# Optimization experiments

Measured on AMD Instinct MI355X. Metric: run time of the kernel, lower is better.

Reference implementation:

```python
import jax, jax.numpy as jnp
import numpy as np
from jax import lax

WINDOW_SIZE = 11
SIGMA = 1.5
CHANNELS = 3
C1 = 0.01 ** 2
C2 = 0.03 ** 2


def _create_window():
    coords = jnp.arange(WINDOW_SIZE, dtype=jnp.float32) - WINDOW_SIZE // 2
    g = jnp.exp(-coords ** 2 / (2.0 * SIGMA ** 2))
    g = g / g.sum()
    w2d = g[:, None] * g[None, :]                      # (11, 11)
    # depthwise kernel, OIHW with groups=channels -> (C, 1, k, k)
    return jnp.broadcast_to(w2d, (CHANNELS, 1, WINDOW_SIZE, WINDOW_SIZE))


def _dwconv(x, window):
    pad = WINDOW_SIZE // 2
    return lax.conv_general_dilated(
        x, window,
        window_strides=(1, 1),
        padding=[(pad, pad), (pad, pad)],
        dimension_numbers=('NCHW', 'OIHW', 'NCHW'),
        feature_group_count=CHANNELS,
    )


def setup_inputs() -> dict:
    key = jax.random.key(0)
    k1, k2 = jax.random.split(key)
    pred = jax.random.uniform(k1, (32, 3, 512, 512), dtype=jnp.float32)
    target = jax.random.uniform(k2, (32, 3, 512, 512), dtype=jnp.float32)
    return {"pred": pred, "target": target}


def reference(pred, target):
    pred = pred.astype(jnp.float32)
    target = target.astype(jnp.float32)
    window = _create_window()

    mu1 = _dwconv(pred, window)
    mu2 = _dwconv(target, window)
    mu1_sq = mu1 * mu1
    mu2_sq = mu2 * mu2
    mu1_mu2 = mu1 * mu2
    sigma1_sq = _dwconv(pred * pred, window) - mu1_sq
    sigma2_sq = _dwconv(target * target, window) - mu2_sq
    sigma12 = _dwconv(pred * target, window) - mu1_mu2

    ssim_map = ((2.0 * mu1_mu2 + C1) * (2.0 * sigma12 + C2)) / (
        (mu1_sq + mu2_sq + C1) * (sigma1_sq + sigma2_sq + C2))
    return 1.0 - ssim_map.mean()
```

## Files before the change

### kernel.cpp

```cpp
#include <hip/hip_runtime.h>
#include <hip/hip_bf16.h>
#include <math.h>

#define BLOCK 256
#define IMG 512
#define SW 88
#define NBLOCKS 3072
#define NACC 128
#define N_TOTAL 25165824.0f

typedef float f32x4 __attribute__((ext_vector_type(4)));
typedef short s16x8 __attribute__((ext_vector_type(8)));
typedef short s16x4 __attribute__((ext_vector_type(4)));

struct WB { unsigned short b[11]; float c2; float k1; float k2; };
union FR  { unsigned int u[4]; s16x8 s; };
union FR2 { unsigned int u[2]; s16x4 s; };

#if __has_builtin(__builtin_amdgcn_mfma_f32_16x16x16bf16_1k)
#define MFMA16(A,B,C) __builtin_amdgcn_mfma_f32_16x16x16bf16_1k((A),(B),(C),0,0,0)
#else
__device__ __forceinline__ f32x4 mfma16_asm(s16x4 a, s16x4 b, f32x4 c) {
    f32x4 d;
    asm("v_mfma_f32_16x16x16_bf16 %0, %1, %2, %3" : "=v"(d) : "v"(a), "v"(b), "v"(c));
    return d;
}
#define MFMA16(A,B,C) mfma16_asm((A),(B),(C))
#endif

#define WG_SYNC() do { \
    asm volatile("s_waitcnt lgkmcnt(0)" ::: "memory"); \
    __builtin_amdgcn_s_barrier(); \
    asm volatile("" ::: "memory"); \
} while (0)

__device__ __forceinline__ unsigned int pk2(float a, float b) {
    union { __hip_bfloat162 h; unsigned int u; } cv;
    cv.h = __float22bfloat162_rn(make_float2(a, b));
    return cv.u;
}

__device__ __forceinline__ void stage4(unsigned short (*sq)[16][SW],
                                       int r, int i, float4 xv, float4 yv) {
    *(uint2*)&sq[0][r][4*i] = make_uint2(pk2(xv.x,xv.y), pk2(xv.z,xv.w));
    *(uint2*)&sq[1][r][4*i] = make_uint2(pk2(yv.x,yv.y), pk2(yv.z,yv.w));
    *(uint2*)&sq[2][r][4*i] = make_uint2(
        pk2(xv.x*xv.x + yv.x*yv.x, xv.y*xv.y + yv.y*yv.y),
        pk2(xv.z*xv.z + yv.z*yv.z, xv.w*xv.w + yv.w*yv.w));
    *(uint2*)&sq[3][r][4*i] = make_uint2(pk2(xv.x*yv.x, xv.y*yv.y),
                                         pk2(xv.z*yv.z, xv.w*yv.w));
}

__device__ __forceinline__ void load_set(const float* __restrict__ P,
                                         const float* __restrict__ T,
                                         int R0, int step,
                                         int rA, int colA, bool okcA,
                                         bool hasB, int rB, int colB, bool okcB,
                                         float4& xA, float4& yA, float4& xB, float4& yB) {
    const int gr = R0 - 5 + 16 * step + rA;
    if (okcA && gr >= 0 && gr < IMG) {
        xA = *(const float4*)(P + ((size_t)gr << 9) + colA);
        yA = *(const float4*)(T + ((size_t)gr << 9) + colA);
    } else { xA = make_float4(0,0,0,0); yA = make_float4(0,0,0,0); }
    const int grB = R0 - 5 + 16 * step + rB;
    if (hasB && okcB && grB >= 0 && grB < IMG) {
        xB = *(const float4*)(P + ((size_t)grB << 9) + colB);
        yB = *(const float4*)(T + ((size_t)grB << 9) + colB);
    } else { xB = make_float4(0,0,0,0); yB = make_float4(0,0,0,0); }
}

#define H_PHASE(CUR, QB)                                                     \
  do {                                                                       \
    FR a0_, a1_, a2_, a3_;                                                   \
    a0_.s = *(const s16x8*)&s_q[QB][0][l15][hoff];                           \
    a1_.s = *(const s16x8*)&s_q[QB][1][l15][hoff];                           \
    a2_.s = *(const s16x8*)&s_q[QB][2][l15][hoff];                           \
    a3_.s = *(const s16x8*)&s_q[QB][3][l15][hoff];                           \
    f32x4 d0_ = __builtin_amdgcn_mfma_f32_16x16x32_bf16(a0_.s, bw.s, z,0,0,0);\
    f32x4 d1_ = __builtin_amdgcn_mfma_f32_16x16x32_bf16(a1_.s, bw.s, z,0,0,0);\
    f32x4 d2_ = __builtin_amdgcn_mfma_f32_16x16x32_bf16(a2_.s, bw.s, z,0,0,0);\
    f32x4 d3_ = __builtin_amdgcn_mfma_f32_16x16x32_bf16(a3_.s, bw.s, z,0,0,0);\
    CUR[0].u[0]=pk2(d0_[0],d0_[1]); CUR[0].u[1]=pk2(d0_[2],d0_[3]);          \
    CUR[1].u[0]=pk2(d1_[0],d1_[1]); CUR[1].u[1]=pk2(d1_[2],d1_[3]);          \
    CUR[2].u[0]=pk2(d2_[0],d2_[1]); CUR[2].u[1]=pk2(d2_[2],d2_[3]);          \
    CUR[3].u[0]=pk2(d3_[0],d3_[1]); CUR[3].u[1]=pk2(d3_[2],d3_[3]);          \
  } while (0)

#define V_PHASE(CUR, PRV)                                                    \
  do {                                                                       \
    f32x4 c0_ = MFMA16(awhi.s, CUR[0].s, z);                                 \
    f32x4 c1_ = MFMA16(awhi.s, CUR[1].s, z);                                 \
    f32x4 c2_ = MFMA16(awhi.s, CUR[2].s, z);                                 \
    f32x4 c3_ = MFMA16(awhi.s, CUR[3].s, z);                                 \
    c0_ = MFMA16(awlo.s, PRV[0].s, c0_);                                     \
    c1_ = MFMA16(awlo.s, PRV[1].s, c1_);                                     \
    c2_ = MFMA16(awlo.s, PRV[2].s, c2_);                                     \
    c3_ = MFMA16(awlo.s, PRV[3].s, c3_);                                     \
    _Pragma("unroll")                                                        \
    for (int i = 0; i < 4; ++i) {                                            \
        const float u1   = c0_[i];                                           \
        const float u2   = c1_[i];                                           \
        const float m11  = u1 * u1;                                          \
        const float m22  = u2 * u2;                                          \
        const float m12  = u1 * u2;                                          \
        const float esum = c2_[i] * c2;                         \
        const float e12  = c3_[i] * c2;                                      \
        const float A_ = fmaf(2.f, m12, K1);                                 \
        const float B_ = fmaf(2.f, e12 - m12, K2);                           \
        const float C_ = m11 + m22 + K1;                                     \
        const float D_ = esum - (m11 + m22) + K2;                            \
        lsum = fmaf(A_ * B_, __builtin_amdgcn_rcpf(C_ * D_), lsum);          \
    }                                                                        \
  } while (0)

#define STEP(S, CUR, PRV, QB)                                                \
  do {                                                                       \
    if ((S) < 8)                                                             \
        load_set(P, T, R0, (S) + 1, rA, colA, okcA, hasB, rB, colB, okcB,    \
                 nxA, nyA, nxB, nyB);                                        \
    H_PHASE(CUR, QB);                                                        \
    if ((S) >= 1) V_PHASE(CUR, PRV);                                         \
    if ((S) < 8) {                                                           \
        stage4(s_q[1 - (QB)], rA, iA, nxA, nyA);                             \
        if (hasB) stage4(s_q[1 - (QB)], rB, iB, nxB, nyB);                   \
        WG_SYNC();                                                           \
    }                                                                        \
  } while (0)

__global__ __launch_bounds__(BLOCK, 3)
void ssim_tiled(const float* __restrict__ pred,
                const float* __restrict__ targ,
                float* __restrict__ accum, WB wb) {
    __shared__ unsigned short s_q[2][4][16][SW];

    const int tid = threadIdx.x;
    const int bx    = blockIdx.x;
    const int plane = bx >> 5;
    const int rem   = bx & 31;
    const int tx    = rem >> 2;
    const int ry    = rem & 3;
    const int C0    = tx * 64;
    const int R0    = ry * 128;

    const float* P = pred + (size_t)plane * (IMG * IMG);
    const float* T = targ + (size_t)plane * (IMG * IMG);

    const int w    = tid >> 6;
    const int lane = tid & 63;
    const int l15  = lane & 15;
    const int quad = lane >> 4;
    const int hoff = 16 * w + 8 * quad;

    const int slotA = w * 80 + lane;
    const int rA = slotA / 20, iA = slotA % 20;
    const int colA = C0 - 8 + 4 * iA;
    const bool okcA = (colA >= 0) && (colA + 4 <= IMG);
    const bool hasB = (lane < 16);
    const int slotB = w * 80 + 64 + l15;
    const int rB = slotB / 20, iB = slotB % 20;
    const int colB = C0 - 8 + 4 * iB;
    const bool okcB = (colB >= 0) && (colB + 4 <= IMG);

    const float c2 = wb.c2, K1 = wb.k1, K2 = wb.k2;
    const f32x4 z = {0.f, 0.f, 0.f, 0.f};
    float lsum = 0.f;

    float4 nxA, nyA, nxB, nyB;
    load_set(P, T, R0, 0, rA, colA, okcA, hasB, rB, colB, okcB, nxA, nyA, nxB, nyB);

    FR bw; FR2 awlo, awhi;
    {
        const int ti = lane & 31;
        int tv = 0;
#pragma unroll
        for (int k = 0; k < 11; ++k) tv = (ti == k) ? (int)wb.b[k] : tv;
        const int tnext = __shfl(tv, (lane + 1) & 63);
        const int pairT = (tv & 0xffff) | (tnext << 16);
        const int base_b = 8 * quad - l15 - 3;
        const int baseL  = 4 * quad - l15;
        const int baseH  = 4 * quad - l15 + 16;
#pragma unroll
        for (int t = 0; t < 4; ++t)
            bw.u[t] = (unsigned int)__shfl(pairT, (base_b + 2 * t) & 63);
#pragma unroll
        for (int t = 0; t < 2; ++t) {
            awlo.u[t] = (unsigned int)__shfl(pairT, (baseL + 2 * t) & 63);
            awhi.u[t] = (unsigned int)__shfl(pairT, (baseH + 2 * t) & 63);
        }
    }

    stage4(s_q[0], rA, iA, nxA, nyA);
    if (hasB) stage4(s_q[0], rB, iB, nxB, nyB);
    WG_SYNC();

    FR2 vbE[4], vbO[4];

    STEP(0, vbE, vbO, 0);
    STEP(1, vbO, vbE, 1);
    STEP(2, vbE, vbO, 0);
    STEP(3, vbO, vbE, 1);
    STEP(4, vbE, vbO, 0);
    STEP(5, vbO, vbE, 1);
    STEP(6, vbE, vbO, 0);
    STEP(7, vbO, vbE, 1);
    STEP(8, vbE, vbO, 0);

#pragma unroll
    for (int off = 32; off > 0; off >>= 1) lsum += __shfl_down(lsum, off, 64);
    if (lane == 0) atomicAdd(&accum[(bx * 4 + w) & (NACC - 1)], lsum);
}

__global__ void ssim_finalize(const float* __restrict__ accum, float* __restrict__ out) {
    const int l = threadIdx.x;
    float v = accum[l] + accum[l + 64];
#pragma unroll
    for (int off = 32; off > 0; off >>= 1) v += __shfl_down(v, off, 64);
    if (l == 0) out[0] = 1.0f - v * (1.0f / N_TOTAL);
}

extern "C" void kernel_launch(void* const* d_in, const int* in_sizes, int n_in,
                              void* d_out, int out_size, void* d_ws, size_t ws_size,
                              hipStream_t stream) {
    const float* pred = (const float*)d_in[0];
    const float* targ = (const float*)d_in[1];
    float* out = (float*)d_out;
    float* ws  = (float*)d_ws;

    WB wb;
    {
        double gg[11], sum = 0.0;
        for (int k = 0; k < 11; ++k) {
            const double d = (double)(k - 5);
            gg[k] = exp(-d * d / 4.5);
            sum += gg[k];
        }
        double sbf = 0.0;
        for (int k = 0; k < 11; ++k) {
            union { float f; unsigned int u; } cv;
            cv.f = (float)(gg[k] / sum);
            const unsigned int r = (cv.u + 0x7fffu + ((cv.u >> 16) & 1u)) >> 16;
            wb.b[k] = (unsigned short)r;
            union { float f; unsigned int u; } bk;
            bk.u = r << 16;
            sbf += (double)bk.f;
        }
        const double s2 = sbf * sbf;
        wb.c2 = (float)s2;
        wb.k1 = (float)(0.0001 * s2 * s2);
        wb.k2 = (float)(0.0009 * s2 * s2);
    }

    hipMemsetAsync(ws, 0, NACC * sizeof(float), stream);
    ssim_tiled<<<NBLOCKS, BLOCK, 0, stream>>>(pred, targ, ws, wb);
    ssim_finalize<<<1, 64, 0, stream>>>(ws, out);
}
```

Baseline: 250.0 us.

## Interleave two independent row streams per block to halve barrier count

Each block's 9-step row sweep is split into two independent 5-step streams (steps 0-4 and 4-8). They are interleaved in the same loop body, using four LDS buffers instead of two and loading two row sets per stage. This halves the number of workgroup barriers and gives the scheduler two independent MFMA chains per phase, which should hide latency better. The cost is one redundant horizontal pass at step 4, double the LDS footprint and more live registers, which could cut occupancy.

Result: no change. 249.6 us (-0.2%).

```diff
diff --git a/kernel.cpp b/kernel.cpp
--- a/kernel.cpp
+++ b/kernel.cpp
@@ -69,13 +69,12 @@
     } else { xB = make_float4(0,0,0,0); yB = make_float4(0,0,0,0); }
 }
 
-#define H_PHASE(CUR, QB)                                                     \
-  do {                                                                       \
+#define H_PHASE(CUR, QI) do {                                                \
     FR a0_, a1_, a2_, a3_;                                                   \
-    a0_.s = *(const s16x8*)&s_q[QB][0][l15][hoff];                           \
-    a1_.s = *(const s16x8*)&s_q[QB][1][l15][hoff];                           \
-    a2_.s = *(const s16x8*)&s_q[QB][2][l15][hoff];                           \
-    a3_.s = *(const s16x8*)&s_q[QB][3][l15][hoff];                           \
+    a0_.s = *(const s16x8*)&s_q[QI][0][l15][hoff];                           \
+    a1_.s = *(const s16x8*)&s_q[QI][1][l15][hoff];                           \
+    a2_.s = *(const s16x8*)&s_q[QI][2][l15][hoff];                           \
+    a3_.s = *(const s16x8*)&s_q[QI][3][l15][hoff];                           \
     f32x4 d0_ = __builtin_amdgcn_mfma_f32_16x16x32_bf16(a0_.s, bw.s, z,0,0,0);\
     f32x4 d1_ = __builtin_amdgcn_mfma_f32_16x16x32_bf16(a1_.s, bw.s, z,0,0,0);\
     f32x4 d2_ = __builtin_amdgcn_mfma_f32_16x16x32_bf16(a2_.s, bw.s, z,0,0,0);\
@@ -84,10 +83,9 @@
     CUR[1].u[0]=pk2(d1_[0],d1_[1]); CUR[1].u[1]=pk2(d1_[2],d1_[3]);          \
     CUR[2].u[0]=pk2(d2_[0],d2_[1]); CUR[2].u[1]=pk2(d2_[2],d2_[3]);          \
     CUR[3].u[0]=pk2(d3_[0],d3_[1]); CUR[3].u[1]=pk2(d3_[2],d3_[3]);          \
-  } while (0)
-
-#define V_PHASE(CUR, PRV)                                                    \
-  do {                                                                       \
+} while (0)
+
+#define V_PHASE(CUR, PRV) do {                                               \
     f32x4 c0_ = MFMA16(awhi.s, CUR[0].s, z);                                 \
     f32x4 c1_ = MFMA16(awhi.s, CUR[1].s, z);                                 \
     f32x4 c2_ = MFMA16(awhi.s, CUR[2].s, z);                                 \
@@ -111,27 +109,27 @@
         const float D_ = esum - (m11 + m22) + K2;                            \
         lsum = fmaf(A_ * B_, __builtin_amdgcn_rcpf(C_ * D_), lsum);          \
     }                                                                        \
-  } while (0)
-
-#define STEP(S, CUR, PRV, QB)                                                \
-  do {                                                                       \
-    if ((S) < 8)                                                             \
-        load_set(P, T, R0, (S) + 1, rA, colA, okcA, hasB, rB, colB, okcB,    \
-                 nxA, nyA, nxB, nyB);                                        \
-    H_PHASE(CUR, QB);                                                        \
-    if ((S) >= 1) V_PHASE(CUR, PRV);                                         \
-    if ((S) < 8) {                                                           \
-        stage4(s_q[1 - (QB)], rA, iA, nxA, nyA);                             \
-        if (hasB) stage4(s_q[1 - (QB)], rB, iB, nxB, nyB);                   \
-        WG_SYNC();                                                           \
-    }                                                                        \
-  } while (0)
+} while (0)
+
+#define STAGE_AB(QIA, QIB) do {                                              \
+    stage4(s_q[QIA], rA, iA, fax, fay);                                      \
+    if (hasB) stage4(s_q[QIA], rB, iB, fbx, fby);                            \
+    stage4(s_q[QIB], rA, iA, gax, gay);                                      \
+    if (hasB) stage4(s_q[QIB], rB, iB, gbx, gby);                            \
+} while (0)
+
+#define LOAD_AB(SA, SB) do {                                                 \
+    load_set(P, T, R0, (SA), rA, colA, okcA, hasB, rB, colB, okcB,           \
+             fax, fay, fbx, fby);                                            \
+    load_set(P, T, R0, (SB), rA, colA, okcA, hasB, rB, colB, okcB,           \
+             gax, gay, gbx, gby);                                            \
+} while (0)
 
 __global__ __launch_bounds__(BLOCK, 3)
 void ssim_tiled(const float* __restrict__ pred,
                 const float* __restrict__ targ,
                 float* __restrict__ accum, WB wb) {
-    __shared__ unsigned short s_q[2][4][16][SW];
+    __shared__ unsigned short s_q[4][4][16][SW];
 
     const int tid = threadIdx.x;
     const int bx    = blockIdx.x;
@@ -165,8 +163,9 @@
     const f32x4 z = {0.f, 0.f, 0.f, 0.f};
     float lsum = 0.f;
 
-    float4 nxA, nyA, nxB, nyB;
-    load_set(P, T, R0, 0, rA, colA, okcA, hasB, rB, colB, okcB, nxA, nyA, nxB, nyB);
+    float4 fax, fay, fbx, fby;
+    float4 gax, gay, gbx, gby;
+    LOAD_AB(0, 4);
 
     FR bw; FR2 awlo, awhi;
     {
@@ -189,21 +188,37 @@
         }
     }
 
-    stage4(s_q[0], rA, iA, nxA, nyA);
-    if (hasB) stage4(s_q[0], rB, iB, nxB, nyB);
-    WG_SYNC();
-
-    FR2 vbE[4], vbO[4];
-
-    STEP(0, vbE, vbO, 0);
-    STEP(1, vbO, vbE, 1);
-    STEP(2, vbE, vbO, 0);
-    STEP(3, vbO, vbE, 1);
-    STEP(4, vbE, vbO, 0);
-    STEP(5, vbO, vbE, 1);
-    STEP(6, vbE, vbO, 0);
-    STEP(7, vbO, vbE, 1);
-    STEP(8, vbE, vbO, 0);
+    STAGE_AB(0, 2);
+    LOAD_AB(1, 5);
+    WG_SYNC();
+
+    FR2 vbAE[4], vbAO[4], vbBE[4], vbBO[4];
+
+    H_PHASE(vbAE, 0);
+    H_PHASE(vbBE, 2);
+    STAGE_AB(1, 3);
+    LOAD_AB(2, 6);
+    WG_SYNC();
+
+    H_PHASE(vbAO, 1);  V_PHASE(vbAO, vbAE);
+    H_PHASE(vbBO, 3);  V_PHASE(vbBO, vbBE);
+    STAGE_AB(0, 2);
+    LOAD_AB(3, 7);
+    WG_SYNC();
+
+    H_PHASE(vbAE, 0);  V_PHASE(vbAE, vbAO);
+    H_PHASE(vbBE, 2);  V_PHASE(vbBE, vbBO);
+    STAGE_AB(1, 3);
+    LOAD_AB(4, 8);
+    WG_SYNC();
+
+    H_PHASE(vbAO, 1);  V_PHASE(vbAO, vbAE);
+    H_PHASE(vbBO, 3);  V_PHASE(vbBO, vbBE);
+    STAGE_AB(0, 2);
+    WG_SYNC();
+
+    H_PHASE(vbAE, 0);  V_PHASE(vbAE, vbAO);
+    H_PHASE(vbBE, 2);  V_PHASE(vbBE, vbBO);
 
 #pragma unroll
     for (int off = 32; off > 0; off >>= 1) lsum += __shfl_down(lsum, off, 64);
```
